# Performance work log

Hardware: AMD Instinct MI355X
Metric: run time of the kernel (lower is better)

The kernel has to match this reference:

```python
import jax, jax.numpy as jnp
import numpy as np

GRID_INTERVAL = 0.3  # grid_interval init arg (used as module-level global in the original source)
EPS = 1e-12
B, G, M, N_ORB, DIM = 16, 4096, 128, 400, 768


def setup_inputs() -> dict:
    key = jax.random.key(0)
    k1, k2, k3, k4, k5 = jax.random.split(key, 5)
    # distances are physical (positive); avoid d=0 so negative powers in the laplace GTO stay finite
    distance_matrices = jax.random.uniform(k1, (B, G, M), jnp.float32, 0.5, 8.0)
    quantum_numbers = jax.random.randint(k2, (B, M), 0, 3).astype(jnp.int32) + 1  # principal q in {1,2,3}
    atomic_orbitals = jax.random.randint(k3, (B, M), 0, N_ORB)
    N_electrons = jax.random.uniform(k4, (B,), jnp.float32, 2.0, 68.0)
    coefficient_table = jax.random.normal(k5, (N_ORB, DIM), jnp.float32)  # nn.Embedding(N_orbitals, dim)
    zeta_table = jnp.ones((N_ORB, 1), jnp.float32)  # nn.Embedding(N_orbitals, 1), init ones
    return dict(distance_matrices=distance_matrices,
                quantum_numbers=quantum_numbers,
                atomic_orbitals=atomic_orbitals,
                N_electrons=N_electrons,
                coefficient_table=coefficient_table,
                zeta_table=zeta_table)


def _gto_bases(d, q, z):
    """GTO and laplace-GTO basis matrices, normalized over the grid axis.
    d: [B,G,M] distances; q: [B,1,M] principal quantum numbers (float); z: [B,1,M] zetas.
    Block-diagonal pad value 1e6 in the original makes off-block entries exactly 0,
    so the per-molecule batched norm over axis=1 matches the block-diagonal column norm.
    """
    e = jnp.exp(-(z ** 2) * d ** 2)
    gto = d ** (q - 1.0) * e  # d^(q-1) * exp(-z^2 d^2)
    denom = jnp.maximum(jnp.linalg.norm(gto, axis=1, keepdims=True), EPS) * GRID_INTERVAL ** 1.5
    l_gto = d ** (q - 3.0) * e * (4.0 * z ** 4 * d ** 4
                                  - 2.0 * z ** 2 * (2.0 * q + 1.0) * d ** 2
                                  + q * (q - 1.0))
    return gto / denom, l_gto / denom


def reference(distance_matrices, quantum_numbers, atomic_orbitals, N_electrons,
              coefficient_table, zeta_table):
    Bv, Gv, Mv = distance_matrices.shape
    D = coefficient_table.shape[1]
    q = quantum_numbers.astype(distance_matrices.dtype)[:, None, :]      # [B,1,M]
    z = zeta_table[atomic_orbitals][..., 0][:, None, :]                  # [B,1,M]
    n_gto, n_l_gto = _gto_bases(distance_matrices, q, z)                 # [B,G,M]
    # LCAO coefficients: F.normalize(coefficient(AOs), 2, 0) per molecule (norm over orbital axis M)
    c = coefficient_table[atomic_orbitals]                               # [B,M,D]
    c = c / jnp.maximum(jnp.linalg.norm(c, axis=1, keepdims=True), EPS)
    mo = jnp.einsum('bgm,bmd->bgd', n_gto, c)                            # molecular orbitals
    l_mo = jnp.einsum('bgm,bmd->bgd', n_l_gto, c)                        # laplace MOs
    # normalize MOs per molecule over the grid axis, scale by sqrt(N_el/dim); laplace MOs share denom
    denom = jnp.maximum(jnp.linalg.norm(mo, axis=1, keepdims=True), EPS)
    scale = jnp.sqrt(N_electrons / D)[:, None, None]
    mo_n = scale * mo / denom
    l_mo_n = scale * l_mo / denom
    # torch.cat over molecules along the grid axis -> [B*G, D]; stack (MOs, laplace MOs)
    return jnp.stack([mo_n.reshape(Bv * Gv, D), l_mo_n.reshape(Bv * Gv, D)])
```

## Files before the change

kernel.cpp:

```cpp
#include <hip/hip_runtime.h>
#include <hip/hip_bf16.h>
#include <math.h>

#define B_    16
#define G_    4096
#define M_    128
#define D_    768
#define GI15  0.16431676725154983f
#define EPS_  1e-12f

typedef __attribute__((ext_vector_type(8))) short short8v;
typedef __attribute__((ext_vector_type(4))) float f32x4;
typedef unsigned short ushort_t;
typedef unsigned int   uint_t;

__device__ __forceinline__ ushort_t f2bf(float f) {
    uint_t u = __float_as_uint(f);
    u += 0x7FFFu + ((u >> 16) & 1u);
    return (ushort_t)(u >> 16);
}
__device__ __forceinline__ float bf2f(ushort_t h) {
    return __uint_as_float(((uint_t)h) << 16);
}

__global__ __launch_bounds__(256) void k_agen(
        const float* __restrict__ dist,
        const int*   __restrict__ qn,
        const int*   __restrict__ ao,
        const float* __restrict__ zeta,
        ushort_t*    __restrict__ A4) {
    const int b = blockIdx.y, gb = blockIdx.x, tid = threadIdx.x;
    const int m = tid & 127, gh2 = tid >> 7;
    const float q  = (float)qn[b * M_ + m];
    const float z  = zeta[ao[b * M_ + m]];
    const float z2 = z * z;
    const float c4 = 4.f * z2 * z2;
    const float c2 = 2.f * z2 * (2.f * q + 1.f);
    const float c0 = q * (q - 1.f);
    const int kc = m >> 5, k = m & 31;
    ushort_t* base = A4 + ((((size_t)(b * 64 + gb)) * 4 + kc) * 4) * 2048 + k;
    const float* dp = dist + ((size_t)(b * G_ + gb * 64 + gh2)) * M_ + m;
    #pragma unroll 4
    for (int r = 0; r < 32; ++r) {
        int g = r * 2 + gh2;
        float d  = dp[(size_t)(r * 2) * M_];
        float d2 = d * d;
        float e  = __expf(-z2 * d2);
        float p1 = (q < 1.5f) ? 1.f : ((q < 2.5f) ? d : d2);
        float gto  = p1 * e;
        float poly = fmaf(fmaf(c4, d2, -c2), d2, c0);
        float lg   = __fdividef(p1, d2) * e * poly;
        ushort_t gh = f2bf(gto);
        ushort_t lh = f2bf(lg);
        ushort_t* p = base + g * 32;
        p[0]    = gh;
        p[2048] = f2bf(gto - bf2f(gh));
        p[4096] = lh;
        p[6144] = f2bf(lg - bf2f(lh));
    }
}

__global__ __launch_bounds__(256) void k_gram_part(
        const float* __restrict__ dist,
        const int*   __restrict__ qn,
        const int*   __restrict__ ao,
        const float* __restrict__ zeta,
        float*       __restrict__ part) {
    __shared__ float sg[64][M_];
    __shared__ float pz2[M_], pq[M_];
    const int b = blockIdx.y, ch = blockIdx.x, tid = threadIdx.x;
    if (tid < M_) {
        pq[tid] = (float)qn[b * M_ + tid];
        float z = zeta[ao[b * M_ + tid]];
        pz2[tid] = z * z;
    }
    __syncthreads();
    {
        int m = tid & 127;
        float z2 = pz2[m], q = pq[m];
        for (int r = tid >> 7; r < 64; r += 2) {
            float d = dist[((size_t)(b * G_ + ch * 64 + r)) * M_ + m];
            float e  = __expf(-z2 * d * d);
            float p1 = (q < 1.5f) ? 1.f : ((q < 2.5f) ? d : d * d);
            sg[r][m] = p1 * e;
        }
    }
    __syncthreads();
    const int mi0 = (tid >> 4) * 8;
    const int mj0 = (tid & 15) * 8;
    float acc[8][8];
    #pragma unroll
    for (int i = 0; i < 8; ++i)
        #pragma unroll
        for (int j = 0; j < 8; ++j) acc[i][j] = 0.f;
    #pragma unroll 2
    for (int g = 0; g < 64; ++g) {
        float av[8], bv[8];
        *(float4*)&av[0] = *(const float4*)&sg[g][mi0];
        *(float4*)&av[4] = *(const float4*)&sg[g][mi0 + 4];
        *(float4*)&bv[0] = *(const float4*)&sg[g][mj0];
        *(float4*)&bv[4] = *(const float4*)&sg[g][mj0 + 4];
        #pragma unroll
        for (int i = 0; i < 8; ++i)
            #pragma unroll
            for (int j = 0; j < 8; ++j)
                acc[i][j] = fmaf(av[i], bv[j], acc[i][j]);
    }
    float* pp = part + ((size_t)(ch * B_ + b)) * (M_ * M_);
    #pragma unroll
    for (int i = 0; i < 8; ++i) {
        *(float4*)&pp[(mi0 + i) * M_ + mj0]     = make_float4(acc[i][0], acc[i][1], acc[i][2], acc[i][3]);
        *(float4*)&pp[(mi0 + i) * M_ + mj0 + 4] = make_float4(acc[i][4], acc[i][5], acc[i][6], acc[i][7]);
    }
}

__global__ void k_gram_red(const float* __restrict__ part,
                           float*       __restrict__ gram) {
    int idx = blockIdx.x * 256 + threadIdx.x;
    float s = 0.f;
    #pragma unroll 8
    for (int ch = 0; ch < 64; ++ch)
        s += part[(size_t)ch * (B_ * M_ * M_) + idx];
    gram[idx] = s;
}

__global__ __launch_bounds__(256) void k_mosq(
        const float* __restrict__ gram,
        const int*   __restrict__ ao,
        const float* __restrict__ table,
        const float* __restrict__ Nel,
        ushort_t*    __restrict__ bhiG,
        ushort_t*    __restrict__ bloG) {
    __shared__ float sv[M_][64];
    __shared__ float sGq[32][M_];
    __shared__ float prg[M_];
    __shared__ float sred[4][64];
    __shared__ float srcn[64], scf[64];
    const int b = blockIdx.y, d0 = blockIdx.x * 64, tid = threadIdx.x;
    const int dl = tid & 63, quad = tid >> 6;
    const float* gb = gram + (size_t)b * M_ * M_;
    if (tid < M_)
        prg[tid] = 1.f / (fmaxf(sqrtf(gb[tid * M_ + tid]), EPS_) * GI15);
    #pragma unroll 4
    for (int k = 0; k < 32; ++k) {
        int m = quad * 32 + k;
        sv[m][dl] = table[(size_t)ao[b * M_ + m] * D_ + d0 + dl];
    }
    __syncthreads();
    {
        float cs = 0.f;
        #pragma unroll 4
        for (int k = 0; k < 32; ++k) { float v = sv[quad * 32 + k][dl]; cs = fmaf(v, v, cs); }
        sred[quad][dl] = cs;
    }
    __syncthreads();
    if (quad == 0)
        srcn[dl] = 1.f / fmaxf(sqrtf(sred[0][dl] + sred[1][dl] + sred[2][dl] + sred[3][dl]), EPS_);
    #pragma unroll 4
    for (int k = 0; k < 32; ++k) { int m = quad * 32 + k; sv[m][dl] *= prg[m]; }
    __syncthreads();
    float acc = 0.f;
    for (int qt = 0; qt < 4; ++qt) {
        for (int e = tid; e < 32 * M_; e += 256)
            sGq[e >> 7][e & 127] = gb[(qt * 32 + (e >> 7)) * M_ + (e & 127)];
        __syncthreads();
        #pragma unroll
        for (int mr8 = 0; mr8 < 8; ++mr8) {
            int mr = quad * 8 + mr8;
            float t0 = 0.f, t1 = 0.f, t2 = 0.f, t3 = 0.f;
            #pragma unroll 4
            for (int mc = 0; mc < M_; mc += 4) {
                t0 = fmaf(sGq[mr][mc],     sv[mc][dl],     t0);
                t1 = fmaf(sGq[mr][mc + 1], sv[mc + 1][dl], t1);
                t2 = fmaf(sGq[mr][mc + 2], sv[mc + 2][dl], t2);
                t3 = fmaf(sGq[mr][mc + 3], sv[mc + 3][dl], t3);
            }
            acc = fmaf(sv[qt * 32 + mr][dl], (t0 + t1) + (t2 + t3), acc);
        }
        __syncthreads();
    }
    sred[quad][dl] = acc;
    __syncthreads();
    if (quad == 0) {
        float qf  = fmaxf(sred[0][dl] + sred[1][dl] + sred[2][dl] + sred[3][dl], 0.f);
        float rcn = srcn[dl];
        float mo  = rcn * sqrtf(qf);
        scf[dl] = sqrtf(Nel[b] / (float)D_) / fmaxf(mo, EPS_) * rcn;
    }
    __syncthreads();
    {
        float cfv = scf[dl];
        ushort_t* bh = bhiG + ((size_t)b * D_ + d0 + dl) * M_;
        ushort_t* bl = bloG + ((size_t)b * D_ + d0 + dl) * M_;
        #pragma unroll
        for (int mq = 0; mq < 4; ++mq) {
            int mb = quad * 32 + mq * 8;
            ushort_t h[8], l[8];
            #pragma unroll
            for (int r = 0; r < 8; ++r) {
                float v = sv[mb + r][dl] * cfv;
                h[r] = f2bf(v);
                l[r] = f2bf(v - bf2f(h[r]));
            }
            *(uint4*)&bh[mb] = *(const uint4*)&h[0];
            *(uint4*)&bl[mb] = *(const uint4*)&l[0];
        }
    }
}

__global__ __launch_bounds__(512, 4) void k_gemm(
        const ushort_t* __restrict__ A4,
        const ushort_t* __restrict__ bhiG,
        const ushort_t* __restrict__ bloG,
        float*       __restrict__ out) {
    __shared__ ushort_t sBh[16384], sBl[16384];
    const int tid = threadIdx.x;
    const int b  = blockIdx.z;
    const int g0 = blockIdx.y * 64;
    const int d0 = blockIdx.x * 128;

    {
        const uint_t* gh = (const uint_t*)(bhiG + ((size_t)b * D_ + d0) * M_);
        const uint_t* gl = (const uint_t*)(bloG + ((size_t)b * D_ + d0) * M_);
        #pragma unroll
        for (int p = 0; p < 16; ++p) {
            int j = p * 512 + tid;
            int drow   = j >> 6;
            int inrow4 = (j & 63) << 2;
            int tgt = drow * 256 + (inrow4 ^ ((drow & 7) << 4));
            *(uint_t*)((char*)sBh + tgt) = gh[j];
            *(uint_t*)((char*)sBl + tgt) = gl[j];
        }
    }

    const int lane = tid & 63, w = tid >> 6;
    const int gsub  = (w & 3) * 16;
    const int dhalf = (w >> 2) * 64;
    const int lrow = lane & 15, lk8 = (lane >> 4) * 8;
    f32x4 accm[4], accl[4];
    #pragma unroll
    for (int t = 0; t < 4; ++t) {
        accm[t] = (f32x4){0.f, 0.f, 0.f, 0.f};
        accl[t] = (f32x4){0.f, 0.f, 0.f, 0.f};
    }
    const ushort_t* Ab = A4 + ((size_t)(b * 64 + blockIdx.y)) * 32768
                            + (gsub + lrow) * 32 + lk8;
    __syncthreads();

    #pragma unroll
    for (int kc = 0; kc < 4; ++kc) {
        const ushort_t* Ak = Ab + kc * 8192;
        short8v agh = *(const short8v*)&Ak[0];
        short8v agl = *(const short8v*)&Ak[2048];
        short8v alh = *(const short8v*)&Ak[4096];
        short8v all_= *(const short8v*)&Ak[6144];
        int kk2 = (kc * 32 + lk8) * 2;
        #pragma unroll
        for (int dt = 0; dt < 4; ++dt) {
            int dr = dhalf + dt * 16 + lrow;
            int off = dr * 256 + (kk2 ^ ((dr & 7) << 4));
            short8v bh = *(const short8v*)((const char*)sBh + off);
            short8v bl = *(const short8v*)((const char*)sBl + off);
            accm[dt] = __builtin_amdgcn_mfma_f32_16x16x32_bf16(agh, bh, accm[dt], 0, 0, 0);
            accm[dt] = __builtin_amdgcn_mfma_f32_16x16x32_bf16(agh, bl, accm[dt], 0, 0, 0);
            accm[dt] = __builtin_amdgcn_mfma_f32_16x16x32_bf16(agl, bh, accm[dt], 0, 0, 0);
            accl[dt] = __builtin_amdgcn_mfma_f32_16x16x32_bf16(alh, bh, accl[dt], 0, 0, 0);
            accl[dt] = __builtin_amdgcn_mfma_f32_16x16x32_bf16(alh, bl, accl[dt], 0, 0, 0);
            accl[dt] = __builtin_amdgcn_mfma_f32_16x16x32_bf16(all_, bh, accl[dt], 0, 0, 0);
        }
    }

    const size_t HALF = (size_t)B_ * G_ * D_;
    const int grow = g0 + gsub + (lane >> 4) * 4;
    #pragma unroll
    for (int dt = 0; dt < 4; ++dt) {
        int dcol = d0 + dhalf + dt * 16 + lrow;
        #pragma unroll
        for (int r = 0; r < 4; ++r) {
            size_t off = ((size_t)(b * G_) + grow + r) * D_ + dcol;
            out[off]        = accm[dt][r];
            out[HALF + off] = accl[dt][r];
        }
    }
}

extern "C" void kernel_launch(void* const* d_in, const int* in_sizes, int n_in,
                              void* d_out, int out_size, void* d_ws, size_t ws_size,
                              hipStream_t stream) {
    const float* dist  = (const float*)d_in[0];
    const int*   qn    = (const int*)  d_in[1];
    const int*   ao    = (const int*)  d_in[2];
    const float* Nel   = (const float*)d_in[3];
    const float* table = (const float*)d_in[4];
    const float* zeta  = (const float*)d_in[5];
    float* out = (float*)d_out;
    char*  wsb = (char*)d_ws;

    float*    gram = (float*)wsb;
    ushort_t* bhi  = (ushort_t*)(wsb + (size_t)(1u << 20));
    ushort_t* blo  = (ushort_t*)(wsb + (size_t)(4u << 20));
    ushort_t* A4   = (ushort_t*)(wsb + (size_t)(8u << 20));
    float*    part = out;

    k_agen<<<dim3(64, B_), 256, 0, stream>>>(dist, qn, ao, zeta, A4);
    k_gram_part<<<dim3(64, B_), 256, 0, stream>>>(dist, qn, ao, zeta, part);
    k_gram_red<<<1024, 256, 0, stream>>>(part, gram);
    k_mosq<<<dim3(D_ / 64, B_), 256, 0, stream>>>(gram, ao, table, Nel, bhi, blo);
    k_gemm<<<dim3(D_ / 128, G_ / 64, B_), 512, 0, stream>>>(A4, bhi, blo, out);
}
```

Baseline: 621.5 us.

## Fuse Gram partial computation into A-generation kernel; prefetch A fragments in GEMM

The partial Gram-matrix kernel is merged into k_agen. The GTO values it already computes are written to shared memory, so the distance matrix is no longer read twice, exp is not recomputed, and one kernel launch is removed. Separately, k_gemm now loads all A fragments into registers before staging B into LDS, so the global A loads overlap with the B copy. In exchange, k_agen uses 32KB of shared memory and a larger register footprint, which may reduce occupancy, and the 16 prefetched A vectors raise register pressure in the GEMM.

```diff
diff --git a/kernel.cpp b/kernel.cpp
--- a/kernel.cpp
+++ b/kernel.cpp
@@ -28,7 +28,9 @@
         const int*   __restrict__ qn,
         const int*   __restrict__ ao,
         const float* __restrict__ zeta,
-        ushort_t*    __restrict__ A4) {
+        ushort_t*    __restrict__ A4,
+        float*       __restrict__ part) {
+    __shared__ float sg[64][M_];
     const int b = blockIdx.y, gb = blockIdx.x, tid = threadIdx.x;
     const int m = tid & 127, gh2 = tid >> 7;
     const float q  = (float)qn[b * M_ + m];
@@ -50,6 +52,7 @@
         float gto  = p1 * e;
         float poly = fmaf(fmaf(c4, d2, -c2), d2, c0);
         float lg   = __fdividef(p1, d2) * e * poly;
+        sg[g][m] = gto;
         ushort_t gh = f2bf(gto);
         ushort_t lh = f2bf(lg);
         ushort_t* p = base + g * 32;
@@ -57,33 +60,6 @@
         p[2048] = f2bf(gto - bf2f(gh));
         p[4096] = lh;
         p[6144] = f2bf(lg - bf2f(lh));
-    }
-}
-
-__global__ __launch_bounds__(256) void k_gram_part(
-        const float* __restrict__ dist,
-        const int*   __restrict__ qn,
-        const int*   __restrict__ ao,
-        const float* __restrict__ zeta,
-        float*       __restrict__ part) {
-    __shared__ float sg[64][M_];
-    __shared__ float pz2[M_], pq[M_];
-    const int b = blockIdx.y, ch = blockIdx.x, tid = threadIdx.x;
-    if (tid < M_) {
-        pq[tid] = (float)qn[b * M_ + tid];
-        float z = zeta[ao[b * M_ + tid]];
-        pz2[tid] = z * z;
-    }
-    __syncthreads();
-    {
-        int m = tid & 127;
-        float z2 = pz2[m], q = pq[m];
-        for (int r = tid >> 7; r < 64; r += 2) {
-            float d = dist[((size_t)(b * G_ + ch * 64 + r)) * M_ + m];
-            float e  = __expf(-z2 * d * d);
-            float p1 = (q < 1.5f) ? 1.f : ((q < 2.5f) ? d : d * d);
-            sg[r][m] = p1 * e;
-        }
     }
     __syncthreads();
     const int mi0 = (tid >> 4) * 8;
@@ -106,7 +82,7 @@
             for (int j = 0; j < 8; ++j)
                 acc[i][j] = fmaf(av[i], bv[j], acc[i][j]);
     }
-    float* pp = part + ((size_t)(ch * B_ + b)) * (M_ * M_);
+    float* pp = part + ((size_t)(gb * B_ + b)) * (M_ * M_);
     #pragma unroll
     for (int i = 0; i < 8; ++i) {
         *(float4*)&pp[(mi0 + i) * M_ + mj0]     = make_float4(acc[i][0], acc[i][1], acc[i][2], acc[i][3]);
@@ -219,6 +195,23 @@
     const int g0 = blockIdx.y * 64;
     const int d0 = blockIdx.x * 128;
 
+    const int lane = tid & 63, w = tid >> 6;
+    const int gsub  = (w & 3) * 16;
+    const int dhalf = (w >> 2) * 64;
+    const int lrow = lane & 15, lk8 = (lane >> 4) * 8;
+
+    const ushort_t* Ab = A4 + ((size_t)(b * 64 + blockIdx.y)) * 32768
+                            + (gsub + lrow) * 32 + lk8;
+    short8v afr[16];
+    #pragma unroll
+    for (int kc = 0; kc < 4; ++kc) {
+        const ushort_t* Ak = Ab + kc * 8192;
+        afr[kc * 4 + 0] = *(const short8v*)&Ak[0];
+        afr[kc * 4 + 1] = *(const short8v*)&Ak[2048];
+        afr[kc * 4 + 2] = *(const short8v*)&Ak[4096];
+        afr[kc * 4 + 3] = *(const short8v*)&Ak[6144];
+    }
+
     {
         const uint_t* gh = (const uint_t*)(bhiG + ((size_t)b * D_ + d0) * M_);
         const uint_t* gl = (const uint_t*)(bloG + ((size_t)b * D_ + d0) * M_);
@@ -233,27 +226,20 @@
         }
     }
 
-    const int lane = tid & 63, w = tid >> 6;
-    const int gsub  = (w & 3) * 16;
-    const int dhalf = (w >> 2) * 64;
-    const int lrow = lane & 15, lk8 = (lane >> 4) * 8;
     f32x4 accm[4], accl[4];
     #pragma unroll
     for (int t = 0; t < 4; ++t) {
         accm[t] = (f32x4){0.f, 0.f, 0.f, 0.f};
         accl[t] = (f32x4){0.f, 0.f, 0.f, 0.f};
     }
-    const ushort_t* Ab = A4 + ((size_t)(b * 64 + blockIdx.y)) * 32768
-                            + (gsub + lrow) * 32 + lk8;
     __syncthreads();
 
     #pragma unroll
     for (int kc = 0; kc < 4; ++kc) {
-        const ushort_t* Ak = Ab + kc * 8192;
-        short8v agh = *(const short8v*)&Ak[0];
-        short8v agl = *(const short8v*)&Ak[2048];
-        short8v alh = *(const short8v*)&Ak[4096];
-        short8v all_= *(const short8v*)&Ak[6144];
+        short8v agh = afr[kc * 4 + 0];
+        short8v agl = afr[kc * 4 + 1];
+        short8v alh = afr[kc * 4 + 2];
+        short8v all_= afr[kc * 4 + 3];
         int kk2 = (kc * 32 + lk8) * 2;
         #pragma unroll
         for (int dt = 0; dt < 4; ++dt) {
@@ -302,8 +288,7 @@
     ushort_t* A4   = (ushort_t*)(wsb + (size_t)(8u << 20));
     float*    part = out;
 
-    k_agen<<<dim3(64, B_), 256, 0, stream>>>(dist, qn, ao, zeta, A4);
-    k_gram_part<<<dim3(64, B_), 256, 0, stream>>>(dist, qn, ao, zeta, part);
+    k_agen<<<dim3(64, B_), 256, 0, stream>>>(dist, qn, ao, zeta, A4, part);
     k_gram_red<<<1024, 256, 0, stream>>>(part, gram);
     k_mosq<<<dim3(D_ / 64, B_), 256, 0, stream>>>(gram, ao, table, Nel, bhi, blo);
     k_gemm<<<dim3(D_ / 128, G_ / 64, B_), 512, 0, stream>>>(A4, bhi, blo, out);
```

After: 592.9 us. 1.05x faster.
